# Kernel tuning notes

Measured on AMD Instinct MI355X. Metric: run time of the kernel, lower is better.

## Reference

```python
import jax, jax.numpy as jnp
import numpy as np
from jax import lax

E = 192      # hidden size
NH = 6       # attention heads
L = 6        # mixer blocks (permutation length)
CO = 256     # merging output channels
KH, KW = 7, 11   # locality window
LOCAL = (False, False, True, True, True, True)
B, H, W = 64, 8, 64


def skew(x, pad_value):
    # shift every row one step right, turning columns into diagonals (torch skew)
    rest = x.shape[:-2]
    Hd, Wd = x.shape[-2], x.shape[-1]
    x = jnp.pad(x, [(0, 0)] * (x.ndim - 1) + [(0, Hd)], constant_values=pad_value)
    x = x.reshape(*rest, -1)[..., : Hd * (Hd + Wd - 1)]
    x = x.reshape(*rest, Hd, Hd + Wd - 1)
    end = (Hd + Wd - 1) - (Wd // 2) + (Wd % 2 - 1)
    return x[..., Wd // 2 : end]


def make_mask(h, w, kh, kw):
    # boolean [h*w, h*w]; True inside the local window (torch: True = NOT allowed)
    m = jnp.ones((h, w, kh, kw), dtype=bool)
    m = m.transpose(0, 2, 1, 3)        # [h, kh, w, kw]
    m = skew(m, 0)                     # [h, kh, w, w]
    m = m.transpose(2, 3, 0, 1)        # [w, w, h, kh]
    m = skew(m, 0)                     # [w, w, h, h]
    m = m.transpose(2, 0, 3, 1)        # [h, w, h, w]
    return m.reshape(h * w, h * w)


def layernorm(x, g, b, eps=1e-5):
    mu = jnp.mean(x, axis=-1, keepdims=True)
    var = jnp.mean((x - mu) ** 2, axis=-1, keepdims=True)
    return (x - mu) / jnp.sqrt(var + eps) * g + b


def mha(x, mask, wi, bi, wo, bo, nh):
    # torch nn.MultiheadAttention (batch_first, self-attn, inference)
    b, s, e = x.shape
    hd = e // nh
    qkv = x @ wi.T + bi                                   # [b, s, 3e]
    q, k, v = jnp.split(qkv, 3, axis=-1)
    to_heads = lambda t: t.reshape(b, s, nh, hd).transpose(0, 2, 1, 3)
    q, k, v = to_heads(q), to_heads(k), to_heads(v)
    scores = jnp.einsum('bhqd,bhkd->bhqk', q, k) / jnp.sqrt(jnp.asarray(hd, x.dtype))
    if mask is not None:
        scores = jnp.where(mask, -jnp.inf, scores)
    attn = jax.nn.softmax(scores, axis=-1)
    out = jnp.einsum('bhqk,bhkd->bhqd', attn, v)
    out = out.transpose(0, 2, 1, 3).reshape(b, s, e)
    return out @ wo.T + bo


def mixer_block(x, mask, wi, bi, wo, bo, g1, b1, g2, b2, wm1, bm1, wm2, bm2):
    x = layernorm(x, g1, b1)
    x = mha(x, mask, wi, bi, wo, bo, NH) + x
    x = layernorm(x, g2, b2)
    h = jax.nn.relu(x @ wm1.T + bm1)
    return h @ wm2.T + bm2 + x


def fvtr_stage(image, in_w, in_b, out_w, out_b, ln1_g, ln1_b, ln2_g, ln2_b,
               w1, b1, w2, b2, conv_w, conv_b, mln_g, mln_b):
    bsz, c, h, w = image.shape
    x = jnp.swapaxes(image, -1, -3).reshape(bsz, w * h, c)   # [B, W*H, C]
    mask = make_mask(h, w, KH, KW)
    for i, loc in enumerate(LOCAL):
        x = mixer_block(x, mask if loc else None,
                        in_w[i], in_b[i], out_w[i], out_b[i],
                        ln1_g[i], ln1_b[i], ln2_g[i], ln2_b[i],
                        w1[i], b1[i], w2[i], b2[i])
    x = jnp.swapaxes(x.reshape(bsz, w, h, c), -1, -3)        # [B, C, H, W]
    # MergingBlock: conv (3,1) stride (2,1) pad (1,0) + channel LayerNorm
    y = lax.conv_general_dilated(x, conv_w, window_strides=(2, 1),
                                 padding=((1, 1), (0, 0)),
                                 dimension_numbers=('NCHW', 'OIHW', 'NCHW'))
    y = y + conv_b[None, :, None, None]
    y = jnp.moveaxis(y, 1, -1)
    y = layernorm(y, mln_g, mln_b)
    return jnp.moveaxis(y, -1, 1)


def setup_inputs() -> dict:
    key = jax.random.key(0)
    ks = jax.random.split(key, 8)
    s = 0.02
    return {
        'image': jax.random.normal(ks[0], (B, E, H, W), jnp.float32),
        'in_w':  s * jax.random.normal(ks[1], (L, 3 * E, E), jnp.float32),
        'in_b':  jnp.zeros((L, 3 * E), jnp.float32),
        'out_w': s * jax.random.normal(ks[2], (L, E, E), jnp.float32),
        'out_b': jnp.zeros((L, E), jnp.float32),
        'ln1_g': jnp.ones((L, E), jnp.float32),
        'ln1_b': jnp.zeros((L, E), jnp.float32),
        'ln2_g': jnp.ones((L, E), jnp.float32),
        'ln2_b': jnp.zeros((L, E), jnp.float32),
        'w1':    s * jax.random.normal(ks[3], (L, 4 * E, E), jnp.float32),
        'b1':    jnp.zeros((L, 4 * E), jnp.float32),
        'w2':    s * jax.random.normal(ks[4], (L, E, 4 * E), jnp.float32),
        'b2':    jnp.zeros((L, E), jnp.float32),
        'conv_w': s * jax.random.normal(ks[5], (CO, E, 3, 1), jnp.float32),
        'conv_b': jnp.zeros((CO,), jnp.float32),
        'mln_g': jnp.ones((CO,), jnp.float32),
        'mln_b': jnp.zeros((CO,), jnp.float32),
    }


def reference(image, in_w, in_b, out_w, out_b, ln1_g, ln1_b, ln2_g, ln2_b,
              w1, b1, w2, b2, conv_w, conv_b, mln_g, mln_b):
    return fvtr_stage(image, in_w, in_b, out_w, out_b, ln1_g, ln1_b, ln2_g, ln2_b,
                      w1, b1, w2, b2, conv_w, conv_b, mln_g, mln_b)
```

## Files before the change

kernel.cpp:

```cpp
#include <hip/hip_runtime.h>
#include <hip/hip_bf16.h>
#include <math.h>

#define Bn   64
#define Ssz  512
#define Ed   192
#define NHd  6
#define HDd  32
#define Ld   6
#define COd  256
#define Himg 8
#define Wimg 64
#define Mrows (Bn*Ssz)

typedef unsigned int  uint;
typedef unsigned short ushort;
using short8 = __attribute__((ext_vector_type(8))) short;
using f32x4  = __attribute__((ext_vector_type(4))) float;

__device__ inline ushort f2b(float f) {
    uint u = __builtin_bit_cast(uint, f);
    u = (u + 0x7FFFu + ((u >> 16) & 1u)) >> 16;
    return (ushort)u;
}

__device__ __forceinline__ float fexp2(float x) {
#if __has_builtin(__builtin_amdgcn_exp2f)
    return __builtin_amdgcn_exp2f(x);
#else
    return exp2f(x);
#endif
}

__device__ __forceinline__ uint cvt_pk_bf16(float a, float b) {
    uint r;
    asm("v_cvt_pk_bf16_f32 %0, %1, %2" : "=v"(r) : "v"(a), "v"(b));
    return r;
}

__device__ __forceinline__ void gload16(const ushort* g, ushort* l, int lane) {
#if __has_builtin(__builtin_amdgcn_global_load_lds)
    __builtin_amdgcn_global_load_lds(
        (const __attribute__((address_space(1))) uint*)g,
        (__attribute__((address_space(3))) uint*)l, 16, 0, 0);
#else
    *(uint4*)(l + (size_t)lane * 8) = *(const uint4*)g;
#endif
}

__global__ __launch_bounds__(256) void cvt_weights(const float* __restrict__ in_w,
                                                   const float* __restrict__ out_w,
                                                   const float* __restrict__ w1,
                                                   const float* __restrict__ w2,
                                                   const float* __restrict__ convw,
                                                   ushort* __restrict__ Wb) {
    int t = blockIdx.x * 256 + threadIdx.x;
    if (t >= 2801664) return;
    float v;
    if (t < 663552)        v = in_w[t];
    else if (t < 884736)   v = out_w[t - 663552];
    else if (t < 1769472)  v = w1[t - 884736];
    else if (t < 2654208) {
        int u = t - 1769472;
        int k = u % 768;
        int ks = k ^ ((((k >> 2) ^ (k >> 3)) & 1) * 12);
        v = w2[u - k + ks];
    } else {
        int u = t - 2654208;
        int co = u / 576, rem = u % 576;
        int kh = rem / Ed, c = rem % Ed;
        v = convw[((size_t)co * Ed + c) * 3 + kh];
    }
    Wb[t] = f2b(v);
}

__global__ __launch_bounds__(256) void reshape_ln(const float* __restrict__ img,
                                                  const float* __restrict__ g,
                                                  const float* __restrict__ bb,
                                                  float* __restrict__ outf,
                                                  ushort* __restrict__ outb) {
    __shared__ float lds[Ed * 65];
    const int b = blockIdx.x >> 3, h = blockIdx.x & 7;
    const int tid = threadIdx.x;
    const float* src = img + ((size_t)b * Ed * Himg + h) * Wimg;
    #pragma unroll
    for (int i = 0; i < 48; ++i) {
        int idx = i * 256 + tid;
        int c = idx >> 6, w = idx & 63;
        lds[c * 65 + w] = src[(size_t)c * 512 + w];
    }
    __syncthreads();

    const int w = tid >> 2, q = tid & 3;
    float vals[48];
    float s = 0.f;
    #pragma unroll
    for (int j = 0; j < 48; ++j) {
        vals[j] = lds[(q * 48 + j) * 65 + w];
        s += vals[j];
    }
    s += __shfl_xor(s, 1); s += __shfl_xor(s, 2);
    float mu = s * (1.f / 192.f);
    float qv = 0.f;
    #pragma unroll
    for (int j = 0; j < 48; ++j) { float d = vals[j] - mu; qv += d * d; }
    qv += __shfl_xor(qv, 1); qv += __shfl_xor(qv, 2);
    float rstd = rsqrtf(qv * (1.f / 192.f) + 1e-5f);

    size_t row = (size_t)b * Ssz + w * Himg + h;
    float*  of = outf + row * Ed + q * 48;
    ushort* ob = outb + row * Ed + q * 48;
    const float* gg = g + q * 48;
    const float* bv = bb + q * 48;
    #pragma unroll
    for (int j = 0; j < 48; ++j) {
        float y = (vals[j] - mu) * rstd * gg[j] + bv[j];
        of[j] = y;
        ob[j] = f2b(y);
    }
}

template<int RELU, int RESID, int OBF, int VOUT>
__global__ __launch_bounds__(256) void gemm_mfma(
    const ushort* __restrict__ A, const ushort* __restrict__ Wt,
    const float* __restrict__ bias, const float* __restrict__ resid,
    float* __restrict__ C, ushort* __restrict__ Cb,
    ushort* __restrict__ qpout, ushort* __restrict__ kpout,
    ushort* __restrict__ vtout,
    int M, int N, int K)
{
    __shared__ __align__(16) ushort As[12288];
    __shared__ __align__(16) ushort Bs[6144];
    const int tid  = threadIdx.x;
    const int lane = tid & 63;
    const int wave = tid >> 6;
    const int wr = wave >> 1, wc = wave & 1;
    const int bm = blockIdx.x * 128;
    const int bn = blockIdx.y * 64;

    const ushort* Ag[6]; ushort* Al[6];
    #pragma unroll
    for (int i = 0; i < 6; ++i) {
        int fa = 4 * i + wave;
        int msub = fa / 3, ksub = fa % 3;
        int m = msub * 16 + (lane & 15);
        int k = ksub * 32 + ((lane >> 4) << 3);
        Ag[i] = A + (size_t)(bm + m) * K + k;
        Al[i] = As + fa * 512;
    }
    const ushort* Bg[3]; ushort* Bl[3];
    #pragma unroll
    for (int i = 0; i < 3; ++i) {
        int fb = 4 * i + wave;
        int nsub = fb / 3, ksub = fb % 3;
        int n = nsub * 16 + (lane & 15);
        int k = ksub * 32 + ((lane >> 4) << 3);
        Bg[i] = Wt + (size_t)(bn + n) * K + k;
        Bl[i] = Bs + fb * 512;
    }

    f32x4 acc[4][2];
    #pragma unroll
    for (int i = 0; i < 4; ++i)
        #pragma unroll
        for (int j = 0; j < 2; ++j) acc[i][j] = (f32x4){0.f, 0.f, 0.f, 0.f};

    for (int k0 = 0; k0 < K; k0 += 96) {
        #pragma unroll
        for (int i = 0; i < 6; ++i) gload16(Ag[i] + k0, Al[i], lane);
        #pragma unroll
        for (int i = 0; i < 3; ++i) gload16(Bg[i] + k0, Bl[i], lane);
        __syncthreads();
        #pragma unroll
        for (int ksub = 0; ksub < 3; ++ksub) {
            short8 af[4], bf[2];
            #pragma unroll
            for (int ms = 0; ms < 4; ++ms)
                af[ms] = *(const short8*)(As + (((wr*4+ms)*3 + ksub) * 64 + lane) * 8);
            #pragma unroll
            for (int ns = 0; ns < 2; ++ns)
                bf[ns] = *(const short8*)(Bs + (((wc*2+ns)*3 + ksub) * 64 + lane) * 8);
            #pragma unroll
            for (int ms = 0; ms < 4; ++ms)
                #pragma unroll
                for (int ns = 0; ns < 2; ++ns)
                    acc[ms][ns] = __builtin_amdgcn_mfma_f32_16x16x32_bf16(
                        af[ms], bf[ns], acc[ms][ns], 0, 0, 0);
        }
        __syncthreads();
    }

    int q = lane >> 4, colL = lane & 15;
    #pragma unroll
    for (int ms = 0; ms < 4; ++ms) {
        #pragma unroll
        for (int ns = 0; ns < 2; ++ns) {
            int row0 = bm + (wr*4 + ms) * 16 + q * 4;
            int col  = bn + (wc*2 + ns) * 16 + colL;
            float bvv = bias[col];
            float v[4];
            #pragma unroll
            for (int r = 0; r < 4; ++r) {
                v[r] = acc[ms][ns][r] + bvv;
                if (RELU) v[r] = fmaxf(v[r], 0.f);
                if (RESID) v[r] += resid[(size_t)(row0 + r) * N + col];
            }
            if (VOUT) {
                int bidx = row0 >> 9, srow = row0 & 511;
                if (col >= 384) {
                    int hh = (col - 384) >> 5, dd = (col - 384) & 31;
                    int sr = srow ^ ((((srow >> 2) ^ (srow >> 3)) & 1) * 12);
                    ushort4 pv;
                    pv.x = f2b(v[0]); pv.y = f2b(v[1]); pv.z = f2b(v[2]); pv.w = f2b(v[3]);
                    *(ushort4*)(vtout + (((size_t)(bidx * NHd + hh) * 32 + dd) << 9) + sr) = pv;
                } else {
                    ushort* dst = (col < 192) ? qpout : kpout;
                    int cc = (col < 192) ? col : col - 192;
                    if (col < 192) {
                        const float c2 = 0.2550547270628364f;
                        #pragma unroll
                        for (int r = 0; r < 4; ++r) v[r] *= c2;
                    }
                    int hh = cc >> 5, dd = cc & 31;
                    ushort* p = dst + ((size_t)(bidx * NHd + hh) << 14) + (size_t)srow * 32 + dd;
                    p[0]  = f2b(v[0]); p[32] = f2b(v[1]);
                    p[64] = f2b(v[2]); p[96] = f2b(v[3]);
                }
            } else {
                #pragma unroll
                for (int r = 0; r < 4; ++r) {
                    if (OBF) Cb[(size_t)(row0 + r) * N + col] = f2b(v[r]);
                    else     C [(size_t)(row0 + r) * N + col] = v[r];
                }
            }
        }
    }
}

template<int KIT>
__global__ __launch_bounds__(256) void gemm_ln(
    const ushort* __restrict__ A, const ushort* __restrict__ Wt,
    const float* __restrict__ bias, const float* __restrict__ resid,
    const float* __restrict__ lng, const float* __restrict__ lnb,
    float* __restrict__ outf, ushort* __restrict__ outb)
{
    __shared__ __align__(16) ushort As[4096];
    __shared__ __align__(16) ushort Bs[12288];
    const int K = KIT * 64;
    const int lane = threadIdx.x & 63;
    const int wave = threadIdx.x >> 6;
    const int g = lane >> 4, ql = lane & 15;
    const int bm = blockIdx.x * 64;

    const ushort* Gp[8]; ushort* Lp[8];
    #pragma unroll
    for (int i = 0; i < 8; ++i) {
        int f = 4 * i + wave;
        if (f < 8) {
            int msub = f >> 1, ksub = f & 1;
            Gp[i] = A + (size_t)(bm + msub * 16 + ql) * K + ksub * 32 + g * 8;
            Lp[i] = As + f * 512;
        } else {
            int fb = f - 8, nsub = fb >> 1, ksub = fb & 1;
            Gp[i] = Wt + (size_t)(nsub * 16 + ql) * K + ksub * 32 + g * 8;
            Lp[i] = Bs + fb * 512;
        }
    }

    f32x4 acc[12];
    #pragma unroll
    for (int i = 0; i < 12; ++i) acc[i] = (f32x4){0.f, 0.f, 0.f, 0.f};

    for (int kc = 0; kc < KIT; ++kc) {
        #pragma unroll
        for (int i = 0; i < 8; ++i) gload16(Gp[i] + kc * 64, Lp[i], lane);
        __syncthreads();
        #pragma unroll
        for (int ksub = 0; ksub < 2; ++ksub) {
            short8 af = *(const short8*)(As + ((wave * 2 + ksub) * 64 + lane) * 8);
            #pragma unroll
            for (int ns = 0; ns < 12; ++ns) {
                short8 bf = *(const short8*)(Bs + ((ns * 2 + ksub) * 64 + lane) * 8);
                acc[ns] = __builtin_amdgcn_mfma_f32_16x16x32_bf16(af, bf, acc[ns], 0, 0, 0);
            }
        }
        __syncthreads();
    }

    float bi[12], gg[12], bb[12];
    #pragma unroll
    for (int ns = 0; ns < 12; ++ns) {
        int col = ns * 16 + ql;
        bi[ns] = bias[col];
        gg[ns] = lng[col]; bb[ns] = lnb[col];
    }
    #pragma unroll
    for (int r = 0; r < 4; ++r) {
        int row = bm + wave * 16 + g * 4 + r;
        float v[12];
        #pragma unroll
        for (int ns = 0; ns < 12; ++ns)
            v[ns] = acc[ns][r] + bi[ns] + resid[(size_t)row * Ed + ns * 16 + ql];
        float s = 0.f;
        #pragma unroll
        for (int ns = 0; ns < 12; ++ns) s += v[ns];
        s += __shfl_xor(s, 1); s += __shfl_xor(s, 2);
        s += __shfl_xor(s, 4); s += __shfl_xor(s, 8);
        float mu = s * (1.f / 192.f);
        float qv = 0.f;
        #pragma unroll
        for (int ns = 0; ns < 12; ++ns) { float d = v[ns] - mu; qv += d * d; }
        qv += __shfl_xor(qv, 1); qv += __shfl_xor(qv, 2);
        qv += __shfl_xor(qv, 4); qv += __shfl_xor(qv, 8);
        float rstd = rsqrtf(qv * (1.f / 192.f) + 1e-5f);
        #pragma unroll
        for (int ns = 0; ns < 12; ++ns) {
            float y = (v[ns] - mu) * rstd * gg[ns] + bb[ns];
            int col = ns * 16 + ql;
            outf[(size_t)row * Ed + col] = y;
            outb[(size_t)row * Ed + col] = f2b(y);
        }
    }
}

template<int MODE>
__global__ __launch_bounds__(256) void fused_mlp(
    const ushort* __restrict__ X, const ushort* __restrict__ W1,
    const float* __restrict__ b1, const ushort* __restrict__ W2k,
    const float* __restrict__ b2, const float* __restrict__ resid,
    const float* __restrict__ lng, const float* __restrict__ lnb,
    float* __restrict__ outf, ushort* __restrict__ outb,
    ushort* __restrict__ a2out)
{
    __shared__ __align__(16) ushort Ws[2][24][512];
    const int lane = threadIdx.x & 63;
    const int wave = threadIdx.x >> 6;
    const int g = lane >> 4, ql = lane & 15;
    const int bm = blockIdx.x * 64;
    const int row16 = bm + wave * 16;
    const f32x4 z = {0.f,0.f,0.f,0.f};

    short8 xf[6];
    #pragma unroll
    for (int ks = 0; ks < 6; ++ks)
        xf[ks] = *(const short8*)(X + (size_t)(row16 + ql) * Ed + ks * 32 + g * 8);

    const ushort* gsrc[6]; ushort* ldst[6]; int strd[6];
    #pragma unroll
    for (int i = 0; i < 6; ++i) {
        int f = 4 * i + wave;
        if (f < 12) {
            int hsub = f / 6, ksub = f % 6;
            gsrc[i] = W1 + (size_t)(hsub * 16 + ql) * Ed + ksub * 32 + g * 8;
            strd[i] = 32 * Ed;
        } else {
            int n2 = f - 12;
            gsrc[i] = W2k + (size_t)(n2 * 16 + ql) * 768 + g * 8;
            strd[i] = 32;
        }
        ldst[i] = &Ws[0][f][0];
    }
    auto STAGE = [&](int c, int b) {
        #pragma unroll
        for (int i = 0; i < 6; ++i)
            gload16(gsrc[i] + (size_t)c * strd[i], ldst[i] + b * 12288, lane);
    };

    f32x4 yacc[12];
    #pragma unroll
    for (int i = 0; i < 12; ++i) yacc[i] = z;

    STAGE(0, 0);
    #pragma unroll
    for (int c = 0; c < 24; ++c) {
        __syncthreads();
        if (c < 23) STAGE(c + 1, (c + 1) & 1);
        const ushort* wb = &Ws[c & 1][0][0];

        float4 bA = *(const float4*)(b1 + c * 32 + 4 * g);
        float4 bB = *(const float4*)(b1 + c * 32 + 16 + 4 * g);

        f32x4 st0 = z, st1 = z;
        #pragma unroll
        for (int ks = 0; ks < 6; ++ks) {
            short8 a0 = *(const short8*)(wb + (size_t)ks * 512 + lane * 8);
            short8 a1 = *(const short8*)(wb + (size_t)(6 + ks) * 512 + lane * 8);
            st0 = __builtin_amdgcn_mfma_f32_16x16x32_bf16(a0, xf[ks], st0, 0, 0, 0);
            st1 = __builtin_amdgcn_mfma_f32_16x16x32_bf16(a1, xf[ks], st1, 0, 0, 0);
        }
        float p8[8];
        p8[0] = fmaxf(st0[0] + bA.x, 0.f);
        p8[1] = fmaxf(st0[1] + bA.y, 0.f);
        p8[2] = fmaxf(st0[2] + bA.z, 0.f);
        p8[3] = fmaxf(st0[3] + bA.w, 0.f);
        p8[4] = fmaxf(st1[0] + bB.x, 0.f);
        p8[5] = fmaxf(st1[1] + bB.y, 0.f);
        p8[6] = fmaxf(st1[2] + bB.z, 0.f);
        p8[7] = fmaxf(st1[3] + bB.w, 0.f);
        uint Au = cvt_pk_bf16(p8[0], p8[1]);
        uint Bu = cvt_pk_bf16(p8[2], p8[3]);
        uint Cu = cvt_pk_bf16(p8[4], p8[5]);
        uint Du = cvt_pk_bf16(p8[6], p8[7]);
        asm("v_permlane32_swap_b32 %0, %1" : "+v"(Au), "+v"(Cu));
        asm("v_permlane32_swap_b32 %0, %1" : "+v"(Bu), "+v"(Du));
        union { uint u[4]; short8 s; } pk;
        pk.u[0] = Au; pk.u[1] = Bu; pk.u[2] = Cu; pk.u[3] = Du;
        short8 pa = pk.s;

        #pragma unroll
        for (int n2 = 0; n2 < 12; ++n2) {
            short8 bfr = *(const short8*)(wb + (size_t)(12 + n2) * 512 + lane * 8);
            yacc[n2] = __builtin_amdgcn_mfma_f32_16x16x32_bf16(pa, bfr, yacc[n2], 0, 0, 0);
        }
    }

    float bi[12], gg[12], bb[12];
    #pragma unroll
    for (int ns = 0; ns < 12; ++ns) {
        int col = ns * 16 + ql;
        bi[ns] = b2[col];
        if (MODE == 1) { gg[ns] = lng[col]; bb[ns] = lnb[col]; }
    }
    #pragma unroll
    for (int r = 0; r < 4; ++r) {
        int row = row16 + g * 4 + r;
        float v[12];
        #pragma unroll
        for (int ns = 0; ns < 12; ++ns)
            v[ns] = yacc[ns][r] + bi[ns] + resid[(size_t)row * Ed + ns * 16 + ql];
        if (MODE == 1) {
            float s = 0.f;
            #pragma unroll
            for (int ns = 0; ns < 12; ++ns) s += v[ns];
            s += __shfl_xor(s, 1); s += __shfl_xor(s, 2);
            s += __shfl_xor(s, 4); s += __shfl_xor(s, 8);
            float mu = s * (1.f / 192.f);
            float qv = 0.f;
            #pragma unroll
            for (int ns = 0; ns < 12; ++ns) { float d = v[ns] - mu; qv += d * d; }
            qv += __shfl_xor(qv, 1); qv += __shfl_xor(qv, 2);
            qv += __shfl_xor(qv, 4); qv += __shfl_xor(qv, 8);
            float rstd = rsqrtf(qv * (1.f / 192.f) + 1e-5f);
            #pragma unroll
            for (int ns = 0; ns < 12; ++ns) {
                float y = (v[ns] - mu) * rstd * gg[ns] + bb[ns];
                int col = ns * 16 + ql;
                outf[(size_t)row * Ed + col] = y;
                outb[(size_t)row * Ed + col] = f2b(y);
            }
        } else {
            int bz = row >> 9, s = row & 511;
            int w = s >> 3, h = s & 7;
            #pragma unroll
            for (int ho = 0; ho < 4; ++ho) {
                int kh = h + 1 - 2 * ho;
                if (kh >= 0 && kh < 3) {
                    size_t r2 = ((size_t)((bz * 4 + ho) * 64 + w)) * 576 + kh * 192;
                    #pragma unroll
                    for (int ns = 0; ns < 12; ++ns)
                        a2out[r2 + ns * 16 + ql] = f2b(v[ns]);
                }
            }
            if (h == 0) {
                size_t r2 = ((size_t)(bz * 4 * 64 + w)) * 576;
                #pragma unroll
                for (int ns = 0; ns < 12; ++ns)
                    a2out[r2 + ns * 16 + ql] = 0;
            }
        }
    }
}

template<int USE_MASK>
__global__ __launch_bounds__(256) void attn_mfma(const ushort* __restrict__ qp,
                                                 const ushort* __restrict__ kp,
                                                 const ushort* __restrict__ vt,
                                                 ushort* __restrict__ att) {
    const int bh = blockIdx.x;
    const int b = bh / NHd, h = bh % NHd;
    const int wave = threadIdx.x >> 6, lane = threadIdx.x & 63;
    const int g = lane >> 4, ql = lane & 15;
    const int qb = blockIdx.y * 128 + wave * 32;

    const ushort* qbase = qp + ((size_t)bh << 14);
    const ushort* kbase = kp + ((size_t)bh << 14);
    const ushort* vbase = vt + ((size_t)bh << 14);
    short8 qf[2];
    #pragma unroll
    for (int t = 0; t < 2; ++t)
        qf[t] = *(const short8*)(qbase + (size_t)(qb + t * 16 + ql) * 32 + g * 8);

    short8 onesf;
    #pragma unroll
    for (int j = 0; j < 8; ++j) onesf[j] = (short)0x3F80;

    uint m0[2], m1[2]; int qh[2];
    if (USE_MASK) {
        #pragma unroll
        for (int t = 0; t < 2; ++t) {
            int qwt = ((qb + t * 16) & 63) + ql;
            qh[t] = (qb + t * 16) >> 6;
            uint a0 = 0, a1 = 0;
            #pragma unroll
            for (int i = 0; i < 8; ++i) {
                int keyl = (i >> 2) * 16 + 4 * g + (i & 3);
                int d0 = keyl - qwt;      d0 = d0 < 0 ? -d0 : d0;
                int d1 = keyl + 32 - qwt; d1 = d1 < 0 ? -d1 : d1;
                if (d0 <= 5) a0 |= (1u << i);
                if (d1 <= 5) a1 |= (1u << i);
            }
            m0[t] = a0; m1[t] = a1;
        }
    }

    f32x4 o0[2], o1[2], o2[2];
    #pragma unroll
    for (int t = 0; t < 2; ++t) {
        o0[t] = (f32x4){0.f,0.f,0.f,0.f};
        o1[t] = (f32x4){0.f,0.f,0.f,0.f};
        o2[t] = (f32x4){0.f,0.f,0.f,0.f};
    }
    const f32x4 z = {0.f,0.f,0.f,0.f};

    short8 kb_[3][2];
    short8 vb_[2][2];
    f32x4  st_[2][4];
    short8 pa[2];

    auto LK = [&](int kt, short8* d) {
        d[0] = *(const short8*)(kbase + (size_t)(kt * 32 + ql) * 32 + g * 8);
        d[1] = *(const short8*)(kbase + (size_t)(kt * 32 + 16 + ql) * 32 + g * 8);
    };
    auto LV = [&](int kt, short8* d) {
        d[0] = *(const short8*)(vbase + (size_t)ql * 512 + kt * 32 + 8 * g);
        d[1] = *(const short8*)(vbase + (size_t)(16 + ql) * 512 + kt * 32 + 8 * g);
    };
    auto S = [&](const short8* k, f32x4* st) {
        st[0] = __builtin_amdgcn_mfma_f32_16x16x32_bf16(k[0], qf[0], z, 0, 0, 0);
        st[1] = __builtin_amdgcn_mfma_f32_16x16x32_bf16(k[1], qf[0], z, 0, 0, 0);
        st[2] = __builtin_amdgcn_mfma_f32_16x16x32_bf16(k[0], qf[1], z, 0, 0, 0);
        st[3] = __builtin_amdgcn_mfma_f32_16x16x32_bf16(k[1], qf[1], z, 0, 0, 0);
    };
    auto F = [&](int kt, const f32x4* st) {
        #pragma unroll
        for (int t = 0; t < 2; ++t) {
            float p8[8];
            #pragma unroll
            for (int r = 0; r < 4; ++r) {
                p8[r]     = fexp2(st[t*2][r]);
                p8[4 + r] = fexp2(st[t*2+1][r]);
            }
            if (USE_MASK) {
                int dh = (kt >> 1) - qh[t]; dh = dh < 0 ? -dh : dh;
                if (dh <= 3) {
                    uint mm = (kt & 1) ? m1[t] : m0[t];
                    #pragma unroll
                    for (int i = 0; i < 8; ++i)
                        if ((mm >> i) & 1u) p8[i] = 0.f;
                }
            }
            uint Au = cvt_pk_bf16(p8[0], p8[1]);
            uint Bu = cvt_pk_bf16(p8[2], p8[3]);
            uint Cu = cvt_pk_bf16(p8[4], p8[5]);
            uint Du = cvt_pk_bf16(p8[6], p8[7]);
            asm("v_permlane32_swap_b32 %0, %1" : "+v"(Au), "+v"(Cu));
            asm("v_permlane32_swap_b32 %0, %1" : "+v"(Bu), "+v"(Du));
            union { uint u[4]; short8 s; } pk;
            pk.u[0] = Au; pk.u[1] = Bu; pk.u[2] = Cu; pk.u[3] = Du;
            pa[t] = pk.s;
        }
    };
    auto PV = [&](const short8* v) {
        #pragma unroll
        for (int t = 0; t < 2; ++t) {
            o0[t] = __builtin_amdgcn_mfma_f32_16x16x32_bf16(pa[t], v[0], o0[t], 0, 0, 0);
            o1[t] = __builtin_amdgcn_mfma_f32_16x16x32_bf16(pa[t], v[1], o1[t], 0, 0, 0);
            o2[t] = __builtin_amdgcn_mfma_f32_16x16x32_bf16(pa[t], onesf, o2[t], 0, 0, 0);
        }
    };

    LK(0, kb_[0]); LK(1, kb_[1]); LK(2, kb_[2]);
    LV(0, vb_[0]); LV(1, vb_[1]);
    S(kb_[0], st_[0]);
    #pragma unroll
    for (int kt = 0; kt < 16; ++kt) {
        if (kt < 15) S(kb_[(kt + 1) % 3], st_[(kt + 1) & 1]);
        if (kt < 13) LK(kt + 3, kb_[kt % 3]);
        F(kt, st_[kt & 1]);
        __builtin_amdgcn_s_setprio(1);
        PV(vb_[kt & 1]);
        __builtin_amdgcn_s_setprio(0);
        if (kt < 14) LV(kt + 2, vb_[kt & 1]);
    }

    ushort* op = att + (size_t)b * Ssz * Ed + h * 32;
    #pragma unroll
    for (int t = 0; t < 2; ++t) {
        #pragma unroll
        for (int r = 0; r < 4; ++r) {
            float iv = 1.f / o2[t][r];
            int row = qb + t * 16 + 4 * g + r;
            op[(size_t)row * Ed + ql]      = f2b(o0[t][r] * iv);
            op[(size_t)row * Ed + 16 + ql] = f2b(o1[t][r] * iv);
        }
    }
}

__global__ __launch_bounds__(256) void ln_out_kernel(const float* __restrict__ C2,
                                                     const float* __restrict__ g,
                                                     const float* __restrict__ beta,
                                                     float* __restrict__ out) {
    __shared__ float lds[32 * 257];
    int w0 = blockIdx.x * 32, ho = blockIdx.y, b = blockIdx.z;
    int tid = threadIdx.x;
    size_t rbase = ((size_t)b * 4 + ho) * 64 + w0;

    for (int i = 0; i < 32; ++i)
        lds[i * 257 + tid] = C2[(rbase + i) * COd + tid];
    __syncthreads();

    int wv = tid >> 6, lane = tid & 63;
    for (int rr = 0; rr < 8; ++rr) {
        int i = wv * 8 + rr;
        float v0 = lds[i*257 + lane], v1 = lds[i*257 + lane + 64];
        float v2 = lds[i*257 + lane + 128], v3 = lds[i*257 + lane + 192];
        float s = v0 + v1 + v2 + v3;
        #pragma unroll
        for (int off = 32; off > 0; off >>= 1) s += __shfl_xor(s, off);
        float mu = s * (1.f / 256.f);
        float d0 = v0-mu, d1 = v1-mu, d2 = v2-mu, d3 = v3-mu;
        float qv = d0*d0 + d1*d1 + d2*d2 + d3*d3;
        #pragma unroll
        for (int off = 32; off > 0; off >>= 1) qv += __shfl_xor(qv, off);
        float rstd = rsqrtf(qv * (1.f / 256.f) + 1e-5f);
        lds[i*257 + lane]       = d0 * rstd * g[lane]       + beta[lane];
        lds[i*257 + lane + 64]  = d1 * rstd * g[lane + 64]  + beta[lane + 64];
        lds[i*257 + lane + 128] = d2 * rstd * g[lane + 128] + beta[lane + 128];
        lds[i*257 + lane + 192] = d3 * rstd * g[lane + 192] + beta[lane + 192];
    }
    __syncthreads();

    int w = tid & 31, half = tid >> 5;
    for (int j = 0; j < 32; ++j) {
        int co = half + j * 8;
        out[(((size_t)b * COd + co) * 4 + ho) * Wimg + w0 + w] = lds[w * 257 + co];
    }
}

extern "C" void kernel_launch(void* const* d_in, const int* in_sizes, int n_in,
                              void* d_out, int out_size, void* d_ws, size_t ws_size,
                              hipStream_t stream) {
    const float* image = (const float*)d_in[0];
    const float* in_w  = (const float*)d_in[1];
    const float* in_b  = (const float*)d_in[2];
    const float* out_w = (const float*)d_in[3];
    const float* out_b = (const float*)d_in[4];
    const float* ln1_g = (const float*)d_in[5];
    const float* ln1_b = (const float*)d_in[6];
    const float* ln2_g = (const float*)d_in[7];
    const float* ln2_b = (const float*)d_in[8];
    const float* w1    = (const float*)d_in[9];
    const float* b1    = (const float*)d_in[10];
    const float* w2    = (const float*)d_in[11];
    const float* b2    = (const float*)d_in[12];
    const float* convw = (const float*)d_in[13];
    const float* convb = (const float*)d_in[14];
    const float* mln_g = (const float*)d_in[15];
    const float* mln_b = (const float*)d_in[16];
    float* out = (float*)d_out;
    float* ws  = (float*)d_ws;

    float* F1   = ws;
    float* F2   = ws + 6291456;
    float* BIG  = ws + 12582912;
    ushort* QP   = (ushort*)BIG;
    ushort* KP   = (ushort*)(BIG + 3145728);
    ushort* VT   = (ushort*)(BIG + 6291456);
    float*  C2   = BIG + 4718592;
    ushort* XNb  = (ushort*)(BIG + 12582912);
    ushort* A2b  = (ushort*)(ws + 25165824);
    ushort* ATTb = (ushort*)(ws + 28311552);
    ushort* Wb   = (ushort*)(ws + 31457280);

    ushort* in_wb  = Wb;
    ushort* out_wb = Wb + 663552;
    ushort* w1b    = Wb + 884736;
    ushort* w2b    = Wb + 1769472;
    ushort* cwb    = Wb + 2654208;

    cvt_weights<<<(2801664 + 255) / 256, 256, 0, stream>>>(
        in_w, out_w, w1, w2, convw, Wb);

    reshape_ln<<<Bn * Himg, 256, 0, stream>>>(image, ln1_g, ln1_b, F1, XNb);

    for (int i = 0; i < Ld; ++i) {
        gemm_mfma<0,0,1,1><<<dim3(Mrows/128, 9), 256, 0, stream>>>(
            XNb, in_wb + (size_t)i * 3*Ed*Ed, in_b + i * 3*Ed,
            nullptr, nullptr, nullptr, QP, KP, VT, Mrows, 3*Ed, Ed);
        if (i >= 2) attn_mfma<1><<<dim3(Bn * NHd, 4), 256, 0, stream>>>(QP, KP, VT, ATTb);
        else        attn_mfma<0><<<dim3(Bn * NHd, 4), 256, 0, stream>>>(QP, KP, VT, ATTb);
        gemm_ln<3><<<Mrows/64, 256, 0, stream>>>(
            ATTb, out_wb + (size_t)i * Ed*Ed, out_b + i*Ed,
            F1, ln2_g + i*Ed, ln2_b + i*Ed, F2, XNb);
        if (i < Ld - 1) {
            fused_mlp<1><<<Mrows/64, 256, 0, stream>>>(
                XNb, w1b + (size_t)i * 4*Ed*Ed, b1 + i * 4*Ed,
                w2b + (size_t)i * 4*Ed*Ed, b2 + i*Ed, F2,
                ln1_g + (i+1)*Ed, ln1_b + (i+1)*Ed, F1, XNb, nullptr);
        } else {
            fused_mlp<2><<<Mrows/64, 256, 0, stream>>>(
                XNb, w1b + (size_t)i * 4*Ed*Ed, b1 + i * 4*Ed,
                w2b + (size_t)i * 4*Ed*Ed, b2 + i*Ed, F2,
                nullptr, nullptr, nullptr, nullptr, A2b);
        }
    }

    gemm_mfma<0,0,0,0><<<dim3(16384/128, 4), 256, 0, stream>>>(
        A2b, cwb, convb, nullptr, C2, nullptr, nullptr, nullptr, nullptr,
        16384, COd, 576);
    ln_out_kernel<<<dim3(2, 4, Bn), 256, 0, stream>>>(C2, mln_g, mln_b, out);
}
```

Before: 938.8 us.

## Triple-buffer fused MLP weights and software-pipeline first GEMM ahead of second

The fused MLP kernel moves from a double-buffered to a triple-buffered LDS weight ring, prefetching two chunks ahead. The first GEMM plus ReLU for chunk c+1 is now issued before the second-GEMM MFMAs of chunk c, so their latencies can overlap. The second GEMM runs at raised wave priority via s_setprio. In exchange, LDS use per block grows by half, which may cut blocks per CU, and more live accumulators raise register pressure.

```diff
diff --git a/kernel.cpp b/kernel.cpp
--- a/kernel.cpp
+++ b/kernel.cpp
@@ -332,7 +332,7 @@
     float* __restrict__ outf, ushort* __restrict__ outb,
     ushort* __restrict__ a2out)
 {
-    __shared__ __align__(16) ushort Ws[2][24][512];
+    __shared__ __align__(16) ushort Ws[3][24][512];
     const int lane = threadIdx.x & 63;
     const int wave = threadIdx.x >> 6;
     const int g = lane >> 4, ql = lane & 15;
@@ -360,7 +360,8 @@
         }
         ldst[i] = &Ws[0][f][0];
     }
-    auto STAGE = [&](int c, int b) {
+    auto STAGE = [&](int c) {
+        int b = c % 3;
         #pragma unroll
         for (int i = 0; i < 6; ++i)
             gload16(gsrc[i] + (size_t)c * strd[i], ldst[i] + b * 12288, lane);
@@ -370,33 +371,33 @@
     #pragma unroll
     for (int i = 0; i < 12; ++i) yacc[i] = z;
 
-    STAGE(0, 0);
-    #pragma unroll
-    for (int c = 0; c < 24; ++c) {
-        __syncthreads();
-        if (c < 23) STAGE(c + 1, (c + 1) & 1);
-        const ushort* wb = &Ws[c & 1][0][0];
-
-        float4 bA = *(const float4*)(b1 + c * 32 + 4 * g);
-        float4 bB = *(const float4*)(b1 + c * 32 + 16 + 4 * g);
-
-        f32x4 st0 = z, st1 = z;
+    f32x4 st_[2][2];
+
+    auto P1 = [&](int c) {
+        const ushort* wb = &Ws[c % 3][0][0];
+        f32x4 s0 = z, s1 = z;
         #pragma unroll
         for (int ks = 0; ks < 6; ++ks) {
             short8 a0 = *(const short8*)(wb + (size_t)ks * 512 + lane * 8);
             short8 a1 = *(const short8*)(wb + (size_t)(6 + ks) * 512 + lane * 8);
-            st0 = __builtin_amdgcn_mfma_f32_16x16x32_bf16(a0, xf[ks], st0, 0, 0, 0);
-            st1 = __builtin_amdgcn_mfma_f32_16x16x32_bf16(a1, xf[ks], st1, 0, 0, 0);
-        }
+            s0 = __builtin_amdgcn_mfma_f32_16x16x32_bf16(a0, xf[ks], s0, 0, 0, 0);
+            s1 = __builtin_amdgcn_mfma_f32_16x16x32_bf16(a1, xf[ks], s1, 0, 0, 0);
+        }
+        st_[c & 1][0] = s0; st_[c & 1][1] = s1;
+    };
+    auto PACK = [&](int c) -> short8 {
+        float4 bA = *(const float4*)(b1 + c * 32 + 4 * g);
+        float4 bB = *(const float4*)(b1 + c * 32 + 16 + 4 * g);
+        const f32x4 s0 = st_[c & 1][0], s1 = st_[c & 1][1];
         float p8[8];
-        p8[0] = fmaxf(st0[0] + bA.x, 0.f);
-        p8[1] = fmaxf(st0[1] + bA.y, 0.f);
-        p8[2] = fmaxf(st0[2] + bA.z, 0.f);
-        p8[3] = fmaxf(st0[3] + bA.w, 0.f);
-        p8[4] = fmaxf(st1[0] + bB.x, 0.f);
-        p8[5] = fmaxf(st1[1] + bB.y, 0.f);
-        p8[6] = fmaxf(st1[2] + bB.z, 0.f);
-        p8[7] = fmaxf(st1[3] + bB.w, 0.f);
+        p8[0] = fmaxf(s0[0] + bA.x, 0.f);
+        p8[1] = fmaxf(s0[1] + bA.y, 0.f);
+        p8[2] = fmaxf(s0[2] + bA.z, 0.f);
+        p8[3] = fmaxf(s0[3] + bA.w, 0.f);
+        p8[4] = fmaxf(s1[0] + bB.x, 0.f);
+        p8[5] = fmaxf(s1[1] + bB.y, 0.f);
+        p8[6] = fmaxf(s1[2] + bB.z, 0.f);
+        p8[7] = fmaxf(s1[3] + bB.w, 0.f);
         uint Au = cvt_pk_bf16(p8[0], p8[1]);
         uint Bu = cvt_pk_bf16(p8[2], p8[3]);
         uint Cu = cvt_pk_bf16(p8[4], p8[5]);
@@ -405,13 +406,29 @@
         asm("v_permlane32_swap_b32 %0, %1" : "+v"(Bu), "+v"(Du));
         union { uint u[4]; short8 s; } pk;
         pk.u[0] = Au; pk.u[1] = Bu; pk.u[2] = Cu; pk.u[3] = Du;
-        short8 pa = pk.s;
-
+        return pk.s;
+    };
+    auto P2 = [&](int c, short8 pa) {
+        const ushort* wb = &Ws[c % 3][0][0];
         #pragma unroll
         for (int n2 = 0; n2 < 12; ++n2) {
             short8 bfr = *(const short8*)(wb + (size_t)(12 + n2) * 512 + lane * 8);
             yacc[n2] = __builtin_amdgcn_mfma_f32_16x16x32_bf16(pa, bfr, yacc[n2], 0, 0, 0);
         }
+    };
+
+    STAGE(0); STAGE(1);
+    __syncthreads();
+    P1(0);
+    #pragma unroll
+    for (int c = 0; c < 24; ++c) {
+        if (c > 0) __syncthreads();
+        if (c < 22) STAGE(c + 2);
+        if (c < 23) P1(c + 1);
+        short8 pa = PACK(c);
+        __builtin_amdgcn_s_setprio(1);
+        P2(c, pa);
+        __builtin_amdgcn_s_setprio(0);
     }
 
     float bi[12], gg[12], bb[12];
```

Result: no change. 925.3 us (-1.4%).

## Double fused MLP row tile to 128 and hidden chunk to 64 for weight reuse

Applied to the files above, without the earlier changes.

The fused MLP kernel now processes 32 rows per wave (128 per block) and stages 64 hidden units per iteration in twice the LDS. Each weight fragment read from LDS feeds two MFMAs, which halves weight traffic per row and halves the number of sync/stage iterations. It also raises wave priority around the second GEMM. In exchange it doubles accumulator registers and LDS, which may reduce occupancy, and halves the grid to 256 blocks, which may underfill the GPU.

```diff
diff --git a/kernel.cpp b/kernel.cpp
--- a/kernel.cpp
+++ b/kernel.cpp
@@ -332,86 +332,104 @@
     float* __restrict__ outf, ushort* __restrict__ outb,
     ushort* __restrict__ a2out)
 {
-    __shared__ __align__(16) ushort Ws[2][24][512];
+    __shared__ __align__(16) ushort Ws[2][48][512];
     const int lane = threadIdx.x & 63;
     const int wave = threadIdx.x >> 6;
     const int g = lane >> 4, ql = lane & 15;
-    const int bm = blockIdx.x * 64;
-    const int row16 = bm + wave * 16;
+    const int bm = blockIdx.x * 128;
+    const int row32 = bm + wave * 32;
     const f32x4 z = {0.f,0.f,0.f,0.f};
 
-    short8 xf[6];
-    #pragma unroll
-    for (int ks = 0; ks < 6; ++ks)
-        xf[ks] = *(const short8*)(X + (size_t)(row16 + ql) * Ed + ks * 32 + g * 8);
-
-    const ushort* gsrc[6]; ushort* ldst[6]; int strd[6];
-    #pragma unroll
-    for (int i = 0; i < 6; ++i) {
-        int f = 4 * i + wave;
-        if (f < 12) {
+    short8 xf[2][6];
+    #pragma unroll
+    for (int rg = 0; rg < 2; ++rg)
+        #pragma unroll
+        for (int ks = 0; ks < 6; ++ks)
+            xf[rg][ks] = *(const short8*)(X + (size_t)(row32 + rg * 16 + ql) * Ed + ks * 32 + g * 8);
+
+    const ushort* gsrc[12]; ushort* ldst[12]; int strd[12];
+    #pragma unroll
+    for (int i = 0; i < 12; ++i) {
+        int f = wave * 12 + i;
+        if (f < 24) {
             int hsub = f / 6, ksub = f % 6;
             gsrc[i] = W1 + (size_t)(hsub * 16 + ql) * Ed + ksub * 32 + g * 8;
-            strd[i] = 32 * Ed;
+            strd[i] = 64 * Ed;
         } else {
-            int n2 = f - 12;
-            gsrc[i] = W2k + (size_t)(n2 * 16 + ql) * 768 + g * 8;
-            strd[i] = 32;
+            int n2 = (f - 24) >> 1, kk = (f - 24) & 1;
+            gsrc[i] = W2k + (size_t)(n2 * 16 + ql) * 768 + kk * 32 + g * 8;
+            strd[i] = 64;
         }
         ldst[i] = &Ws[0][f][0];
     }
-    auto STAGE = [&](int c, int b) {
-        #pragma unroll
-        for (int i = 0; i < 6; ++i)
-            gload16(gsrc[i] + (size_t)c * strd[i], ldst[i] + b * 12288, lane);
+    auto STAGE = [&](int c) {
+        int b = c & 1;
+        #pragma unroll
+        for (int i = 0; i < 12; ++i)
+            gload16(gsrc[i] + (size_t)c * strd[i], ldst[i] + b * 24576, lane);
     };
 
-    f32x4 yacc[12];
-    #pragma unroll
-    for (int i = 0; i < 12; ++i) yacc[i] = z;
-
-    STAGE(0, 0);
-    #pragma unroll
-    for (int c = 0; c < 24; ++c) {
+    f32x4 yacc[2][12];
+    #pragma unroll
+    for (int rg = 0; rg < 2; ++rg)
+        #pragma unroll
+        for (int i = 0; i < 12; ++i) yacc[rg][i] = z;
+
+    auto HALF = [&](int c, int h) {
+        const ushort* wb = &Ws[c & 1][0][0];
+        f32x4 s0[2] = {z, z}, s1[2] = {z, z};
+        #pragma unroll
+        for (int ks = 0; ks < 6; ++ks) {
+            short8 w0  = *(const short8*)(wb + (size_t)((2*h)   * 6 + ks) * 512 + lane * 8);
+            short8 w1f = *(const short8*)(wb + (size_t)((2*h+1) * 6 + ks) * 512 + lane * 8);
+            #pragma unroll
+            for (int rg = 0; rg < 2; ++rg) {
+                s0[rg] = __builtin_amdgcn_mfma_f32_16x16x32_bf16(w0,  xf[rg][ks], s0[rg], 0, 0, 0);
+                s1[rg] = __builtin_amdgcn_mfma_f32_16x16x32_bf16(w1f, xf[rg][ks], s1[rg], 0, 0, 0);
+            }
+        }
+        float4 bA = *(const float4*)(b1 + c * 64 + h * 32 + 4 * g);
+        float4 bB = *(const float4*)(b1 + c * 64 + h * 32 + 16 + 4 * g);
+        short8 pa[2];
+        #pragma unroll
+        for (int rg = 0; rg < 2; ++rg) {
+            float p8[8];
+            p8[0] = fmaxf(s0[rg][0] + bA.x, 0.f);
+            p8[1] = fmaxf(s0[rg][1] + bA.y, 0.f);
+            p8[2] = fmaxf(s0[rg][2] + bA.z, 0.f);
+            p8[3] = fmaxf(s0[rg][3] + bA.w, 0.f);
+            p8[4] = fmaxf(s1[rg][0] + bB.x, 0.f);
+            p8[5] = fmaxf(s1[rg][1] + bB.y, 0.f);
+            p8[6] = fmaxf(s1[rg][2] + bB.z, 0.f);
+            p8[7] = fmaxf(s1[rg][3] + bB.w, 0.f);
+            uint Au = cvt_pk_bf16(p8[0], p8[1]);
+            uint Bu = cvt_pk_bf16(p8[2], p8[3]);
+            uint Cu = cvt_pk_bf16(p8[4], p8[5]);
+            uint Du = cvt_pk_bf16(p8[6], p8[7]);
+            asm("v_permlane32_swap_b32 %0, %1" : "+v"(Au), "+v"(Cu));
+            asm("v_permlane32_swap_b32 %0, %1" : "+v"(Bu), "+v"(Du));
+            union { uint u[4]; short8 s; } pk;
+            pk.u[0] = Au; pk.u[1] = Bu; pk.u[2] = Cu; pk.u[3] = Du;
+            pa[rg] = pk.s;
+        }
+        __builtin_amdgcn_s_setprio(1);
+        #pragma unroll
+        for (int n2 = 0; n2 < 12; ++n2) {
+            short8 bfr = *(const short8*)(wb + (size_t)(24 + n2 * 2 + h) * 512 + lane * 8);
+            #pragma unroll
+            for (int rg = 0; rg < 2; ++rg)
+                yacc[rg][n2] = __builtin_amdgcn_mfma_f32_16x16x32_bf16(pa[rg], bfr, yacc[rg][n2], 0, 0, 0);
+        }
+        __builtin_amdgcn_s_setprio(0);
+    };
+
+    STAGE(0);
+    #pragma unroll
+    for (int c = 0; c < 12; ++c) {
         __syncthreads();
-        if (c < 23) STAGE(c + 1, (c + 1) & 1);
-        const ushort* wb = &Ws[c & 1][0][0];
-
-        float4 bA = *(const float4*)(b1 + c * 32 + 4 * g);
-        float4 bB = *(const float4*)(b1 + c * 32 + 16 + 4 * g);
-
-        f32x4 st0 = z, st1 = z;
-        #pragma unroll
-        for (int ks = 0; ks < 6; ++ks) {
-            short8 a0 = *(const short8*)(wb + (size_t)ks * 512 + lane * 8);
-            short8 a1 = *(const short8*)(wb + (size_t)(6 + ks) * 512 + lane * 8);
-            st0 = __builtin_amdgcn_mfma_f32_16x16x32_bf16(a0, xf[ks], st0, 0, 0, 0);
-            st1 = __builtin_amdgcn_mfma_f32_16x16x32_bf16(a1, xf[ks], st1, 0, 0, 0);
-        }
-        float p8[8];
-        p8[0] = fmaxf(st0[0] + bA.x, 0.f);
-        p8[1] = fmaxf(st0[1] + bA.y, 0.f);
-        p8[2] = fmaxf(st0[2] + bA.z, 0.f);
-        p8[3] = fmaxf(st0[3] + bA.w, 0.f);
-        p8[4] = fmaxf(st1[0] + bB.x, 0.f);
-        p8[5] = fmaxf(st1[1] + bB.y, 0.f);
-        p8[6] = fmaxf(st1[2] + bB.z, 0.f);
-        p8[7] = fmaxf(st1[3] + bB.w, 0.f);
-        uint Au = cvt_pk_bf16(p8[0], p8[1]);
-        uint Bu = cvt_pk_bf16(p8[2], p8[3]);
-        uint Cu = cvt_pk_bf16(p8[4], p8[5]);
-        uint Du = cvt_pk_bf16(p8[6], p8[7]);
-        asm("v_permlane32_swap_b32 %0, %1" : "+v"(Au), "+v"(Cu));
-        asm("v_permlane32_swap_b32 %0, %1" : "+v"(Bu), "+v"(Du));
-        union { uint u[4]; short8 s; } pk;
-        pk.u[0] = Au; pk.u[1] = Bu; pk.u[2] = Cu; pk.u[3] = Du;
-        short8 pa = pk.s;
-
-        #pragma unroll
-        for (int n2 = 0; n2 < 12; ++n2) {
-            short8 bfr = *(const short8*)(wb + (size_t)(12 + n2) * 512 + lane * 8);
-            yacc[n2] = __builtin_amdgcn_mfma_f32_16x16x32_bf16(pa, bfr, yacc[n2], 0, 0, 0);
-        }
+        if (c < 11) STAGE(c + 1);
+        HALF(c, 0);
+        HALF(c, 1);
     }
 
     float bi[12], gg[12], bb[12];
@@ -422,50 +440,53 @@
         if (MODE == 1) { gg[ns] = lng[col]; bb[ns] = lnb[col]; }
     }
     #pragma unroll
-    for (int r = 0; r < 4; ++r) {
-        int row = row16 + g * 4 + r;
-        float v[12];
-        #pragma unroll
-        for (int ns = 0; ns < 12; ++ns)
-            v[ns] = yacc[ns][r] + bi[ns] + resid[(size_t)row * Ed + ns * 16 + ql];
-        if (MODE == 1) {
-            float s = 0.f;
-            #pragma unroll
-            for (int ns = 0; ns < 12; ++ns) s += v[ns];
-            s += __shfl_xor(s, 1); s += __shfl_xor(s, 2);
-            s += __shfl_xor(s, 4); s += __shfl_xor(s, 8);
-            float mu = s * (1.f / 192.f);
-            float qv = 0.f;
-            #pragma unroll
-            for (int ns = 0; ns < 12; ++ns) { float d = v[ns] - mu; qv += d * d; }
-            qv += __shfl_xor(qv, 1); qv += __shfl_xor(qv, 2);
-            qv += __shfl_xor(qv, 4); qv += __shfl_xor(qv, 8);
-            float rstd = rsqrtf(qv * (1.f / 192.f) + 1e-5f);
-            #pragma unroll
-            for (int ns = 0; ns < 12; ++ns) {
-                float y = (v[ns] - mu) * rstd * gg[ns] + bb[ns];
-                int col = ns * 16 + ql;
-                outf[(size_t)row * Ed + col] = y;
-                outb[(size_t)row * Ed + col] = f2b(y);
-            }
-        } else {
-            int bz = row >> 9, s = row & 511;
-            int w = s >> 3, h = s & 7;
-            #pragma unroll
-            for (int ho = 0; ho < 4; ++ho) {
-                int kh = h + 1 - 2 * ho;
-                if (kh >= 0 && kh < 3) {
-                    size_t r2 = ((size_t)((bz * 4 + ho) * 64 + w)) * 576 + kh * 192;
+    for (int rg = 0; rg < 2; ++rg) {
+        #pragma unroll
+        for (int r = 0; r < 4; ++r) {
+            int row = row32 + rg * 16 + g * 4 + r;
+            float v[12];
+            #pragma unroll
+            for (int ns = 0; ns < 12; ++ns)
+                v[ns] = yacc[rg][ns][r] + bi[ns] + resid[(size_t)row * Ed + ns * 16 + ql];
+            if (MODE == 1) {
+                float s = 0.f;
+                #pragma unroll
+                for (int ns = 0; ns < 12; ++ns) s += v[ns];
+                s += __shfl_xor(s, 1); s += __shfl_xor(s, 2);
+                s += __shfl_xor(s, 4); s += __shfl_xor(s, 8);
+                float mu = s * (1.f / 192.f);
+                float qv = 0.f;
+                #pragma unroll
+                for (int ns = 0; ns < 12; ++ns) { float d = v[ns] - mu; qv += d * d; }
+                qv += __shfl_xor(qv, 1); qv += __shfl_xor(qv, 2);
+                qv += __shfl_xor(qv, 4); qv += __shfl_xor(qv, 8);
+                float rstd = rsqrtf(qv * (1.f / 192.f) + 1e-5f);
+                #pragma unroll
+                for (int ns = 0; ns < 12; ++ns) {
+                    float y = (v[ns] - mu) * rstd * gg[ns] + bb[ns];
+                    int col = ns * 16 + ql;
+                    outf[(size_t)row * Ed + col] = y;
+                    outb[(size_t)row * Ed + col] = f2b(y);
+                }
+            } else {
+                int bz = row >> 9, s = row & 511;
+                int w = s >> 3, h = s & 7;
+                #pragma unroll
+                for (int ho = 0; ho < 4; ++ho) {
+                    int kh = h + 1 - 2 * ho;
+                    if (kh >= 0 && kh < 3) {
+                        size_t r2 = ((size_t)((bz * 4 + ho) * 64 + w)) * 576 + kh * 192;
+                        #pragma unroll
+                        for (int ns = 0; ns < 12; ++ns)
+                            a2out[r2 + ns * 16 + ql] = f2b(v[ns]);
+                    }
+                }
+                if (h == 0) {
+                    size_t r2 = ((size_t)(bz * 4 * 64 + w)) * 576;
                     #pragma unroll
                     for (int ns = 0; ns < 12; ++ns)
-                        a2out[r2 + ns * 16 + ql] = f2b(v[ns]);
+                        a2out[r2 + ns * 16 + ql] = 0;
                 }
-            }
-            if (h == 0) {
-                size_t r2 = ((size_t)(bz * 4 * 64 + w)) * 576;
-                #pragma unroll
-                for (int ns = 0; ns < 12; ++ns)
-                    a2out[r2 + ns * 16 + ql] = 0;
             }
         }
     }
@@ -703,12 +724,12 @@
             ATTb, out_wb + (size_t)i * Ed*Ed, out_b + i*Ed,
             F1, ln2_g + i*Ed, ln2_b + i*Ed, F2, XNb);
         if (i < Ld - 1) {
-            fused_mlp<1><<<Mrows/64, 256, 0, stream>>>(
+            fused_mlp<1><<<Mrows/128, 256, 0, stream>>>(
                 XNb, w1b + (size_t)i * 4*Ed*Ed, b1 + i * 4*Ed,
                 w2b + (size_t)i * 4*Ed*Ed, b2 + i*Ed, F2,
                 ln1_g + (i+1)*Ed, ln1_b + (i+1)*Ed, F1, XNb, nullptr);
         } else {
-            fused_mlp<2><<<Mrows/64, 256, 0, stream>>>(
+            fused_mlp<2><<<Mrows/128, 256, 0, stream>>>(
                 XNb, w1b + (size_t)i * 4*Ed*Ed, b1 + i * 4*Ed,
                 w2b + (size_t)i * 4*Ed*Ed, b2 + i*Ed, F2,
                 nullptr, nullptr, nullptr, nullptr, A2b);
```

After: 1.163 ms. +23.9%, slower.
